# Optimization experiments

Measured on AMD Instinct MI355X. Metric: run time of the kernel, lower is better.

## Reference

```python
import jax, jax.numpy as jnp
import numpy as np

B, K_SLOTS, P = 4096, 8, 768
SLOT = P // 3          # 256, slot feature dim
HID = 256              # pres/up hidden width
NC, NP = 512, 512
LN_EPS = 1e-5


def _layernorm(x, g, b):
    m = jnp.mean(x, axis=-1, keepdims=True)
    v = jnp.var(x, axis=-1, keepdims=True)
    return (x - m) * jax.lax.rsqrt(v + LN_EPS) * g + b


def _mlp2(x, W1, b1, g, bt, W2, b2):
    # Linear -> LayerNorm -> ReLU -> Linear (torchvision ops.MLP with hidden=[256, out])
    h = jax.nn.relu(_layernorm(x @ W1 + b1, g, bt))
    return h @ W2 + b2


def setup_inputs() -> dict:
    key = jax.random.key(0)
    ks = jax.random.split(key, 24)
    rn = lambda k, shp, s=1.0: jax.random.normal(k, shp, dtype=jnp.float32) * s
    d = {
        "inst_embed": rn(ks[0], (B, P)),
        "slots": rn(ks[1], (B, K_SLOTS, SLOT)),
        # fc / fp: single Linear(p, p)
        "Wfc": rn(ks[2], (P, P), 1.0 / np.sqrt(P)),
        "bfc": jnp.zeros((P,), jnp.float32),
        "Wfp": rn(ks[3], (P, P), 1.0 / np.sqrt(P)),
        "bfp": jnp.zeros((P,), jnp.float32),
        # memory codebooks (plain randn per the original)
        "Kc": rn(ks[4], (NC, P)),
        "Vc": rn(ks[5], (NC, P)),
        "Kp": rn(ks[6], (NP, P)),
        "Vp": rn(ks[7], (NP, P)),
        # pres MLP: Linear(4p/3,256)+LN+ReLU, Linear(256,p/3)
        "pres_W1": rn(ks[8], (SLOT + P, HID), 1.0 / np.sqrt(SLOT + P)),
        "pres_b1": jnp.zeros((HID,), jnp.float32),
        "pres_g": jnp.ones((HID,), jnp.float32),
        "pres_bt": jnp.zeros((HID,), jnp.float32),
        "pres_W2": rn(ks[9], (HID, SLOT), 1.0 / np.sqrt(HID)),
        "pres_b2": jnp.zeros((SLOT,), jnp.float32),
        # up MLP: same shapes
        "up_W1": rn(ks[10], (SLOT + P, HID), 1.0 / np.sqrt(SLOT + P)),
        "up_b1": jnp.zeros((HID,), jnp.float32),
        "up_g": jnp.ones((HID,), jnp.float32),
        "up_bt": jnp.zeros((HID,), jnp.float32),
        "up_W2": rn(ks[11], (HID, SLOT), 1.0 / np.sqrt(HID)),
        "up_b2": jnp.zeros((SLOT,), jnp.float32),
    }
    return d


def reference(inst_embed, slots, Wfc, bfc, Wfp, bfp, Kc, Vc, Kp, Vp,
              pres_W1, pres_b1, pres_g, pres_bt, pres_W2, pres_b2,
              up_W1, up_b1, up_g, up_bt, up_W2, up_b2):
    scale = jnp.float32(np.sqrt(P))
    # selection: soft attention over the two codebooks
    Qc = inst_embed @ Wfc + bfc                     # [B, P]
    Qp = inst_embed @ Wfp + bfp                     # [B, P]
    c = jax.nn.softmax(jnp.einsum('bi,ci->bc', Qc, Kc) / scale, axis=-1) @ Vc  # [B, P]
    p = jax.nn.softmax(jnp.einsum('bi,pi->bp', Qp, Kp) / scale, axis=-1) @ Vp  # [B, P]
    # update: vectorized over the K slot loop of the original
    cb = jnp.broadcast_to(c[:, None, :], (B, K_SLOTS, P))
    pb = jnp.broadcast_to(p[:, None, :], (B, K_SLOTS, P))
    hc = jnp.concatenate([slots, cb], axis=-1)      # [B, K, SLOT+P]
    hp = jnp.concatenate([slots, pb], axis=-1)      # [B, K, SLOT+P]
    gate_pres = _mlp2(hc, pres_W1, pres_b1, pres_g, pres_bt, pres_W2, pres_b2)
    gate_up = _mlp2(hp, up_W1, up_b1, up_g, up_bt, up_W2, up_b2)
    return slots + gate_pres * gate_up              # [B, K, SLOT]
```

## Files before the change

kernel.cpp:

```cpp
#include <hip/hip_runtime.h>
#include <stdint.h>

#define BB    4096
#define KS    8
#define PP    768
#define SLOT  256
#define HID   256
#define NC    512
#define BKROWS (BB*KS)
typedef unsigned short u16;
typedef short bf16x8 __attribute__((ext_vector_type(8)));
typedef float f32x4  __attribute__((ext_vector_type(4)));

__device__ __forceinline__ u16 f2bf(float x) {
  union { float f; uint32_t u; } v; v.f = x;
  return (u16)((v.u + 0x7FFFu + ((v.u >> 16) & 1u)) >> 16);
}

__device__ __forceinline__ u16 f2h(float x) {
  union { _Float16 h; u16 u; } cv; cv.h = (_Float16)x; return cv.u;
}
__device__ __forceinline__ float h2f(u16 x) {
  union { u16 u; _Float16 h; } cv; cv.u = x; return (float)cv.h;
}

__device__ __forceinline__ void gload_lds16(u16* ldst, const u16* gsrc) {
  __builtin_amdgcn_global_load_lds(
      (const __attribute__((address_space(1))) void*)gsrc,
      (__attribute__((address_space(3))) void*)ldst, 16, 0, 0);
}

template<int EPI>
__device__ __forceinline__ void gemm_core6464(
    const u16* __restrict__ A, int lda,
    const u16* __restrict__ B, int ldb,
    const float* __restrict__ bias,
    void* __restrict__ out, int ldo, int K,
    int blockRow, int blockCol, u16* lsA, u16* lsB)
{
  const int tid  = threadIdx.x;
  const int w    = tid >> 6;
  const int lane = tid & 63;
  const int wm   = w >> 1, wn = w & 1;
  const int rl   = lane >> 4, cl = lane & 15;

  f32x4 acc[2][2];
  const f32x4 zero = {0.f, 0.f, 0.f, 0.f};
#pragma unroll
  for (int i = 0; i < 2; ++i)
#pragma unroll
    for (int j = 0; j < 2; ++j) acc[i][j] = zero;

  const u16* Ablk = A + (size_t)blockRow * lda;
  const u16* Bblk = B + (size_t)blockCol * ldb;

  for (int k0 = 0; k0 < K; k0 += 64) {
#pragma unroll
    for (int i = 0; i < 2; ++i) {
      int seg   = i * 4 + w;
      int off16 = seg * 64 + lane;
      int row   = off16 >> 3;
      int chunk = (off16 & 7) ^ (row & 7);
      gload_lds16(lsA + seg * 512, Ablk + (size_t)row * lda + k0 + chunk * 8);
    }
#pragma unroll
    for (int i = 0; i < 2; ++i) {
      int seg   = i * 4 + w;
      int off16 = seg * 64 + lane;
      int row   = off16 >> 3;
      int chunk = (off16 & 7) ^ (row & 7);
      gload_lds16(lsB + seg * 512, Bblk + (size_t)row * ldb + k0 + chunk * 8);
    }
    __syncthreads();

#pragma unroll
    for (int ks = 0; ks < 2; ++ks) {
      bf16x8 aF[2], bF[2];
#pragma unroll
      for (int f = 0; f < 2; ++f) {
        int r  = wm * 32 + f * 16 + cl;
        int ca = ((ks * 4 + rl) ^ (r & 7)) * 8;
        aF[f] = *(const bf16x8*)(lsA + r * 64 + ca);
        int rn = wn * 32 + f * 16 + cl;
        int cb = ((ks * 4 + rl) ^ (rn & 7)) * 8;
        bF[f] = *(const bf16x8*)(lsB + rn * 64 + cb);
      }
#pragma unroll
      for (int fm = 0; fm < 2; ++fm)
#pragma unroll
        for (int fn = 0; fn < 2; ++fn)
          acc[fm][fn] = __builtin_amdgcn_mfma_f32_16x16x32_bf16(
              aF[fm], bF[fn], acc[fm][fn], 0, 0, 0);
    }
    __syncthreads();
  }

#pragma unroll
  for (int fm = 0; fm < 2; ++fm) {
#pragma unroll
    for (int fn = 0; fn < 2; ++fn) {
      f32x4 v = acc[fm][fn];
#pragma unroll
      for (int r = 0; r < 4; ++r) {
        int grow = blockRow + wm * 32 + fm * 16 + rl * 4 + r;
        int gcol = blockCol + wn * 32 + fn * 16 + cl;
        float x = v[r];
        if constexpr (EPI == 2) {
          ((u16*)out)[(size_t)grow * ldo + gcol] = f2bf(x);
        } else if constexpr (EPI == 3) {
          x += bias[gcol];
          ((float*)out)[(size_t)grow * ldo + gcol] = x;
        } else if constexpr (EPI == 5) {
          x += bias[gcol];
          ((u16*)out)[(size_t)grow * ldo + gcol] = f2h(x);
        }
      }
    }
  }
}

__device__ __forceinline__ void cvt_seg(const float* __restrict__ in,
                                        u16* __restrict__ outp, int b, int n4) {
  int i = b * 256 + threadIdx.x;
  if (i < n4) {
    float4 v = ((const float4*)in)[i];
    ushort4 o;
    o.x = f2bf(v.x); o.y = f2bf(v.y); o.z = f2bf(v.z); o.w = f2bf(v.w);
    ((ushort4*)outp)[i] = o;
  }
}

__device__ __forceinline__ void pack_seg(const float* __restrict__ s0,
                                         const float* __restrict__ s1,
                                         u16* __restrict__ dst, int b) {
  int br = b >> 4, ng = b & 15;
  const float* src = br ? s1 : s0;
  int w = threadIdx.x >> 6, lane = threadIdx.x & 63;
  int rl = lane >> 4, cl = lane & 15;
#pragma unroll
  for (int s = 0; s < 2; ++s) {
    int step = w * 2 + s;
    union { u16 u[8]; uint4 q; } o;
#pragma unroll
    for (int j = 0; j < 8; ++j)
      o.u[j] = f2bf(src[(size_t)(step * 32 + rl * 8 + j) * 256 + ng * 16 + cl]);
    *(uint4*)(dst + (size_t)(((br * 16 + ng) * 8 + step) * 64 + lane) * 8) = o.q;
  }
}

__global__ __launch_bounds__(256) void prep_all(
    const float* __restrict__ inst, const float* __restrict__ Kc,
    const float* __restrict__ Kp, const float* __restrict__ Wfc,
    const float* __restrict__ Wfp, const float* __restrict__ Vc,
    const float* __restrict__ Vp, const float* __restrict__ pW1,
    const float* __restrict__ uW1, const float* __restrict__ pW2,
    const float* __restrict__ uW2, const float* __restrict__ bfc,
    const float* __restrict__ bfp,
    u16* instb, u16* Kcb, u16* Kpb, u16* Wfcb, u16* Wfpb, u16* Vcb, u16* Vpb,
    u16* W1Tp, u16* W1Tu, u16* W1pk, u16* W2pk, float* sb)
{
  __shared__ float tile[32][33];
  int b = blockIdx.x;
  if (b < 3072)      { cvt_seg(inst, instb, b,        786432); return; }
  else if (b < 3456) { cvt_seg(Kc,   Kcb,   b - 3072,  98304); return; }
  else if (b < 3840) { cvt_seg(Kp,   Kpb,   b - 3456,  98304); return; }
  else if (b < 4416) { cvt_seg(Wfc,  Wfcb,  b - 3840, 147456); return; }
  else if (b < 4992) { cvt_seg(Wfp,  Wfpb,  b - 4416, 147456); return; }
  else if (b < 5376) { cvt_seg(Vc,   Vcb,   b - 4992,  98304); return; }
  else if (b < 5760) { cvt_seg(Vp,   Vpb,   b - 5376,  98304); return; }
  else if (b < 6272) {
    int bb = b - 5760;
    const float* in = (bb < 256) ? pW1 : uW1;
    u16* outp = (bb < 256) ? W1Tp : W1Tu;
    bb &= 255;
    int tc = (bb & 7) * 32, tr = (bb >> 3) * 32;
    int lx = threadIdx.x & 31, ly = threadIdx.x >> 5;
#pragma unroll
    for (int i = 0; i < 32; i += 8)
      tile[ly + i][lx] = in[(size_t)(tr + ly + i) * 256 + tc + lx];
    __syncthreads();
#pragma unroll
    for (int i = 0; i < 32; i += 8)
      outp[(size_t)(tc + ly + i) * 1024 + tr + lx] = f2bf(tile[lx][ly + i]);
    return;
  }
  else if (b < 6304) { pack_seg(pW1, uW1, W1pk, b - 6272); return; }
  else if (b < 6336) { pack_seg(pW2, uW2, W2pk, b - 6304); return; }
  else {
    int w = threadIdx.x >> 6, lane = threadIdx.x & 63;
    int row = (b - 6336) * 4 + w;
    int br = row >> 9, n = row & 511;
    const float* Kr = (br ? Kp : Kc) + (size_t)n * PP;
    const float* bf = br ? bfp : bfc;
    float s = 0.f;
#pragma unroll
    for (int j = 0; j < 12; ++j) s += Kr[lane + j * 64] * bf[lane + j * 64];
#pragma unroll
    for (int o = 32; o; o >>= 1) s += __shfl_xor(s, o);
    if (!lane) sb[row] = s;
  }
}

__global__ __launch_bounds__(256) void gemm_mixed(
    const u16* Kcb, const u16* Kpb, const u16* Wfcb, const u16* Wfpb,
    u16* KWc, u16* KWp,
    const u16* W1Tp, const u16* W1Tu, const u16* Vcb, const u16* Vpb,
    u16* VW1p, u16* VW1u)
{
  __shared__ u16 lsA[64 * 64];
  __shared__ u16 lsB[64 * 64];
  int b = blockIdx.x;
  if (b < 192) {
    int z = b / 96, r = b % 96;
    gemm_core6464<2>(z ? Kpb : Kcb, PP, z ? Wfpb : Wfcb, PP, nullptr,
                     z ? KWp : KWc, PP, PP, (r & 7) * 64, (r >> 3) * 64, lsA, lsB);
  } else {
    int c = b - 192, z = c / 32, r = c % 32;
    gemm_core6464<2>((z ? W1Tu : W1Tp) + 256, 1024, z ? Vpb : Vcb, PP, nullptr,
                     z ? VW1u : VW1p, NC, PP, (r & 3) * 64, (r >> 2) * 64, lsA, lsB);
  }
}

__global__ __launch_bounds__(256) void gemm_scores(
    const u16* instb, const u16* KW, const float* sb, u16* scH)
{
  __shared__ u16 lsA[64 * 64];
  __shared__ u16 lsB[64 * 64];
  gemm_core6464<5>(instb, PP, KW, PP, sb, scH, 1024, PP,
                   blockIdx.x * 64, blockIdx.y * 64, lsA, lsB);
}

__global__ __launch_bounds__(256) void gemm_t(
    const u16* Pb, const u16* VW1p, const u16* VW1u,
    const float* pb1, const float* ub1, float* t0, float* t1)
{
  __shared__ u16 lsA[64 * 64];
  __shared__ u16 lsB[64 * 64];
  int z = blockIdx.z;
  gemm_core6464<3>(Pb + (size_t)z * BB * NC, NC, z ? VW1u : VW1p, NC,
                   z ? ub1 : pb1, z ? t1 : t0, SLOT, NC,
                   blockIdx.x * 64, blockIdx.y * 64, lsA, lsB);
}

__global__ __launch_bounds__(256) void softmax_rows(const u16* __restrict__ scH,
                                                    u16* __restrict__ Pp) {
  int w = threadIdx.x >> 6, lane = threadIdx.x & 63;
  int row = blockIdx.x * 4 + w;
  int i = row >> 1, b = row & 1;
  const u16* src = scH + (size_t)i * 1024 + b * 512 + lane * 8;
  uint4 q = *(const uint4*)src;
  const u16* hp = (const u16*)&q;
  float vv[8];
#pragma unroll
  for (int j = 0; j < 8; ++j) vv[j] = h2f(hp[j]);
  float m = vv[0];
#pragma unroll
  for (int j = 1; j < 8; ++j) m = fmaxf(m, vv[j]);
#pragma unroll
  for (int o = 32; o; o >>= 1) m = fmaxf(m, __shfl_xor(m, o));
  const float alpha = 0.03608439182435161f;
  float e[8], s = 0.f;
#pragma unroll
  for (int j = 0; j < 8; ++j) { e[j] = __expf((vv[j] - m) * alpha); s += e[j]; }
#pragma unroll
  for (int o = 32; o; o >>= 1) s += __shfl_xor(s, o);
  float inv = 1.f / s;
  union { u16 u[8]; uint4 q; } ou;
#pragma unroll
  for (int j = 0; j < 8; ++j) ou.u[j] = f2bf(e[j] * inv);
  *(uint4*)(Pp + ((size_t)b * BB + i) * 512 + lane * 8) = ou.q;
}

__global__ __launch_bounds__(512, 4) void fused_update(
    const float* __restrict__ slots,
    const float* __restrict__ t0, const float* __restrict__ t1,
    const u16* __restrict__ W1pk, const u16* __restrict__ W2pk,
    const float* __restrict__ pg, const float* __restrict__ pbt,
    const float* __restrict__ ug, const float* __restrict__ ubt,
    const float* __restrict__ pb2, const float* __restrict__ ub2,
    float* __restrict__ outp)
{
  __shared__ u16 lsH[2][32 * 256];
  __shared__ float lstat[2][32][16];
  __shared__ float lfin[2][32][2];

  const int tid = threadIdx.x, w = tid >> 6, lane = tid & 63;
  const int rl = lane >> 4, cl = lane & 15;
  const int blockRow = blockIdx.x * 32;

  u16* lsA = lsH[0];

#pragma unroll
  for (int it = 0; it < 4; ++it) {
    int L = it * 512 + tid;
    int row = L >> 6, qc = L & 63;
    float4 v = *(const float4*)(slots + (size_t)(blockRow + row) * 256 + qc * 4);
    ushort4 b; b.x = f2bf(v.x); b.y = f2bf(v.y); b.z = f2bf(v.z); b.w = f2bf(v.w);
    int chunk = qc >> 1, half = qc & 1;
    *(ushort4*)(lsA + row * 256 + (((chunk ^ (row & 7)) << 3) + half * 4)) = b;
  }

  float tp_[2][2], tu_[2][2];
#pragma unroll
  for (int fm = 0; fm < 2; ++fm) {
    size_t trr = (size_t)(blockIdx.x * 4 + fm * 2 + (rl >> 1)) * 256;
#pragma unroll
    for (int fn = 0; fn < 2; ++fn) {
      int col = w * 32 + fn * 16 + cl;
      tp_[fm][fn] = t0[trr + col];
      tu_[fm][fn] = t1[trr + col];
    }
  }

#define MF(A, B, C) C = __builtin_amdgcn_mfma_f32_16x16x32_bf16(A, B, C, 0, 0, 0);

  bf16x8 pb[3][2], ub[3][2];
#define FR1(NG, S) (*(const bf16x8*)(W1pk + (size_t)(((NG) * 8 + (S)) * 64 + lane) * 8))
#define LDW1(SL, S) { pb[SL][0] = FR1(w * 2, S);      pb[SL][1] = FR1(w * 2 + 1, S);  \
                      ub[SL][0] = FR1(16 + w * 2, S); ub[SL][1] = FR1(17 + w * 2, S); \
                      asm volatile("" ::: "memory"); }
  LDW1(0, 0) LDW1(1, 1) LDW1(2, 2)
  __syncthreads();

  f32x4 acc[2][4];
  const f32x4 zero = {0.f, 0.f, 0.f, 0.f};
#pragma unroll
  for (int i = 0; i < 2; ++i)
#pragma unroll
    for (int j = 0; j < 4; ++j) acc[i][j] = zero;

#pragma unroll
  for (int s = 0; s < 8; ++s) {
    const int sl = s % 3;
    bf16x8 a0 = *(const bf16x8*)(lsA + cl * 256 + (((s * 4 + rl) ^ (cl & 7)) << 3));
    bf16x8 a1 = *(const bf16x8*)(lsA + (16 + cl) * 256 + (((s * 4 + rl) ^ (cl & 7)) << 3));
    MF(a0, pb[sl][0], acc[0][0]) MF(a1, pb[sl][0], acc[1][0])
    MF(a0, pb[sl][1], acc[0][1]) MF(a1, pb[sl][1], acc[1][1])
    MF(a0, ub[sl][0], acc[0][2]) MF(a1, ub[sl][0], acc[1][2])
    MF(a0, ub[sl][1], acc[0][3]) MF(a1, ub[sl][1], acc[1][3])
    if (s < 5) LDW1(sl, s + 3)
  }
#undef LDW1
#undef FR1

#pragma unroll
  for (int fm = 0; fm < 2; ++fm)
#pragma unroll
    for (int fn = 0; fn < 2; ++fn)
#pragma unroll
      for (int r = 0; r < 4; ++r) {
        acc[fm][fn][r]     += tp_[fm][fn];
        acc[fm][2 + fn][r] += tu_[fm][fn];
      }

#pragma unroll
  for (int fm = 0; fm < 2; ++fm)
#pragma unroll
    for (int br = 0; br < 2; ++br) {
      f32x4 s = acc[fm][br * 2] + acc[fm][br * 2 + 1];
      f32x4 q = acc[fm][br * 2] * acc[fm][br * 2] + acc[fm][br * 2 + 1] * acc[fm][br * 2 + 1];
#pragma unroll
      for (int o = 1; o < 16; o <<= 1) {
#pragma unroll
        for (int r = 0; r < 4; ++r) {
          s[r] += __shfl_xor(s[r], o);
          q[r] += __shfl_xor(q[r], o);
        }
      }
      if (cl == 0) {
#pragma unroll
        for (int r = 0; r < 4; ++r) {
          int row = fm * 16 + rl * 4 + r;
          lstat[br][row][w]     = s[r];
          lstat[br][row][8 + w] = q[r];
        }
      }
    }
  __syncthreads();

  if (tid < 64) {
    int fb = tid >> 5, row = tid & 31;
    f32x4 a = *(const f32x4*)&lstat[fb][row][0];
    f32x4 b = *(const f32x4*)&lstat[fb][row][4];
    f32x4 c = *(const f32x4*)&lstat[fb][row][8];
    f32x4 d = *(const f32x4*)&lstat[fb][row][12];
    float ss = a[0] + a[1] + a[2] + a[3] + b[0] + b[1] + b[2] + b[3];
    float qq = c[0] + c[1] + c[2] + c[3] + d[0] + d[1] + d[2] + d[3];
    float mu = ss * (1.f / 256.f);
    lfin[fb][row][0] = mu;
    lfin[fb][row][1] = rsqrtf(qq * (1.f / 256.f) - mu * mu + 1e-5f);
  }
  __syncthreads();

  bf16x8 qp[3][2], qu[3][2];
#define FR2(NG, S) (*(const bf16x8*)(W2pk + (size_t)(((NG) * 8 + (S)) * 64 + lane) * 8))
#define LDW2(SL, S) { qp[SL][0] = FR2(w * 2, S);      qp[SL][1] = FR2(w * 2 + 1, S);  \
                      qu[SL][0] = FR2(16 + w * 2, S); qu[SL][1] = FR2(17 + w * 2, S); \
                      asm volatile("" ::: "memory"); }
  LDW2(0, 0)

  float b2p[2], b2u[2];
#pragma unroll
  for (int fn = 0; fn < 2; ++fn) {
    int col = w * 32 + fn * 16 + cl;
    b2p[fn] = pb2[col]; b2u[fn] = ub2[col];
  }

  {
    float gv[2][2], btv[2][2];
#pragma unroll
    for (int fn = 0; fn < 2; ++fn) {
      int col = w * 32 + fn * 16 + cl;
      gv[0][fn] = pg[col];  btv[0][fn] = pbt[col];
      gv[1][fn] = ug[col];  btv[1][fn] = ubt[col];
    }
#pragma unroll
    for (int fm = 0; fm < 2; ++fm) {
      float mean[2][4], rstd[2][4];
#pragma unroll
      for (int r = 0; r < 4; ++r) {
        int row = fm * 16 + rl * 4 + r;
        mean[0][r] = lfin[0][row][0]; rstd[0][r] = lfin[0][row][1];
        mean[1][r] = lfin[1][row][0]; rstd[1][r] = lfin[1][row][1];
      }
#pragma unroll
      for (int br = 0; br < 2; ++br)
#pragma unroll
        for (int fn = 0; fn < 2; ++fn) {
          int col = w * 32 + fn * 16 + cl;
#pragma unroll
          for (int r = 0; r < 4; ++r) {
            int row = fm * 16 + rl * 4 + r;
            float h = fmaxf((acc[fm][br * 2 + fn][r] - mean[br][r]) * rstd[br][r]
                            * gv[br][fn] + btv[br][fn], 0.f);
            lsH[br][row * 256 + (((col >> 3) ^ (row & 7)) << 3) + (col & 7)] = f2bf(h);
          }
        }
    }
  }
#pragma unroll
  for (int i = 0; i < 2; ++i)
#pragma unroll
    for (int j = 0; j < 4; ++j) acc[i][j] = zero;
  __syncthreads();

  LDW2(1, 1) LDW2(2, 2)
#pragma unroll
  for (int s = 0; s < 8; ++s) {
    const int sl = s % 3;
    bf16x8 aP0 = *(const bf16x8*)(lsH[0] + cl * 256 + (((s * 4 + rl) ^ (cl & 7)) << 3));
    bf16x8 aP1 = *(const bf16x8*)(lsH[0] + (16 + cl) * 256 + (((s * 4 + rl) ^ (cl & 7)) << 3));
    bf16x8 aU0 = *(const bf16x8*)(lsH[1] + cl * 256 + (((s * 4 + rl) ^ (cl & 7)) << 3));
    bf16x8 aU1 = *(const bf16x8*)(lsH[1] + (16 + cl) * 256 + (((s * 4 + rl) ^ (cl & 7)) << 3));
    MF(aP0, qp[sl][0], acc[0][0]) MF(aP1, qp[sl][0], acc[1][0])
    MF(aP0, qp[sl][1], acc[0][1]) MF(aP1, qp[sl][1], acc[1][1])
    MF(aU0, qu[sl][0], acc[0][2]) MF(aU1, qu[sl][0], acc[1][2])
    MF(aU0, qu[sl][1], acc[0][3]) MF(aU1, qu[sl][1], acc[1][3])
    if (s < 5) LDW2(sl, s + 3)
  }
#undef LDW2
#undef FR2
#undef MF

#pragma unroll
  for (int fm = 0; fm < 2; ++fm)
#pragma unroll
    for (int fn = 0; fn < 2; ++fn)
#pragma unroll
      for (int r = 0; r < 4; ++r) {
        float gp = acc[fm][fn][r]     + b2p[fn];
        float gu = acc[fm][2 + fn][r] + b2u[fn];
        int row = blockRow + fm * 16 + rl * 4 + r;
        int col = w * 32 + fn * 16 + cl;
        size_t idx = (size_t)row * 256 + col;
        outp[idx] = slots[idx] + gp * gu;
      }
}

extern "C" void kernel_launch(void* const* d_in, const int* in_sizes, int n_in,
                              void* d_out, int out_size, void* d_ws, size_t ws_size,
                              hipStream_t stream) {
  const float* inst  = (const float*)d_in[0];
  const float* slots = (const float*)d_in[1];
  const float* Wfc   = (const float*)d_in[2];
  const float* bfc   = (const float*)d_in[3];
  const float* Wfp   = (const float*)d_in[4];
  const float* bfp   = (const float*)d_in[5];
  const float* Kc    = (const float*)d_in[6];
  const float* Vc    = (const float*)d_in[7];
  const float* Kp    = (const float*)d_in[8];
  const float* Vp    = (const float*)d_in[9];
  const float* pW1   = (const float*)d_in[10];
  const float* pb1   = (const float*)d_in[11];
  const float* pg    = (const float*)d_in[12];
  const float* pbt   = (const float*)d_in[13];
  const float* pW2   = (const float*)d_in[14];
  const float* pb2   = (const float*)d_in[15];
  const float* uW1   = (const float*)d_in[16];
  const float* ub1   = (const float*)d_in[17];
  const float* ug    = (const float*)d_in[18];
  const float* ubt   = (const float*)d_in[19];
  const float* uW2   = (const float*)d_in[20];
  const float* ub2   = (const float*)d_in[21];
  float* out = (float*)d_out;
  char*  ws  = (char*)d_ws;

  const size_t OFF_INST  = 0;
  const size_t OFF_KC    = OFF_INST  + 6291456;
  const size_t OFF_KP    = OFF_KC    + 786432;
  const size_t OFF_WFCB  = OFF_KP    + 786432;
  const size_t OFF_WFPB  = OFF_WFCB  + 1179648;
  const size_t OFF_VCB   = OFF_WFPB  + 1179648;
  const size_t OFF_VPB   = OFF_VCB   + 786432;
  const size_t OFF_W1TP  = OFF_VPB   + 786432;
  const size_t OFF_W1TU  = OFF_W1TP  + 524288;
  const size_t OFF_W1PK  = OFF_W1TU  + 524288;
  const size_t OFF_W2PK  = OFF_W1PK  + 262144;
  const size_t OFF_KW    = OFF_W2PK  + 262144;
  const size_t OFF_VW1   = OFF_KW    + 1572864;
  const size_t OFF_SB    = OFF_VW1   + 524288;
  const size_t OFF_T     = OFF_SB    + 4096;
  const size_t OFF_SC    = OFF_T     + 8388608;
  const size_t OFF_P     = OFF_SC    + 8388608;

  u16*   instb = (u16*)(ws + OFF_INST);
  u16*   Kcb   = (u16*)(ws + OFF_KC);
  u16*   Kpb   = (u16*)(ws + OFF_KP);
  u16*   Wfcb  = (u16*)(ws + OFF_WFCB);
  u16*   Wfpb  = (u16*)(ws + OFF_WFPB);
  u16*   Vcb   = (u16*)(ws + OFF_VCB);
  u16*   Vpb   = (u16*)(ws + OFF_VPB);
  u16*   W1Tp  = (u16*)(ws + OFF_W1TP);
  u16*   W1Tu  = (u16*)(ws + OFF_W1TU);
  u16*   W1pk  = (u16*)(ws + OFF_W1PK);
  u16*   W2pk  = (u16*)(ws + OFF_W2PK);
  u16*   KWc   = (u16*)(ws + OFF_KW);
  u16*   KWp   = KWc + (size_t)NC * PP;
  u16*   VW1p  = (u16*)(ws + OFF_VW1);
  u16*   VW1u  = VW1p + (size_t)SLOT * NC;
  float* sb    = (float*)(ws + OFF_SB);
  float* t0    = (float*)(ws + OFF_T);
  float* t1    = t0 + (size_t)BB * SLOT;
  u16*   scH   = (u16*)(ws + OFF_SC);
  u16*   Pb    = (u16*)(ws + OFF_P);

  prep_all<<<dim3(6592), 256, 0, stream>>>(
      inst, Kc, Kp, Wfc, Wfp, Vc, Vp, pW1, uW1, pW2, uW2, bfc, bfp,
      instb, Kcb, Kpb, Wfcb, Wfpb, Vcb, Vpb, W1Tp, W1Tu, W1pk, W2pk, sb);

  gemm_mixed<<<dim3(256), 256, 0, stream>>>(
      Kcb, Kpb, Wfcb, Wfpb, KWc, KWp, W1Tp, W1Tu, Vcb, Vpb, VW1p, VW1u);

  gemm_scores<<<dim3(64, 16), 256, 0, stream>>>(instb, KWc, sb, scH);

  softmax_rows<<<dim3(2048), 256, 0, stream>>>(scH, Pb);

  gemm_t<<<dim3(64, 4, 2), 256, 0, stream>>>(Pb, VW1p, VW1u, pb1, ub1, t0, t1);

  fused_update<<<dim3(1024), 512, 0, stream>>>(
      slots, t0, t1, W1pk, W2pk, pg, pbt, ug, ubt, pb2, ub2, out);

  (void)in_sizes; (void)n_in; (void)out_size; (void)ws_size;
}
```

Before: 92.40 us.

## Split second MLP GEMM by branch across warps and combine gates via LDS

In the second-layer GEMM, each warp now handles one branch (pres or up) over 64 output columns instead of both branches over 32 columns. Each warp therefore reads A fragments from a single hidden buffer, which halves the LDS A-reads per MFMA. Pres-branch warps then write biased results to shared memory, and up-branch warps read them to form the gated residual output. This adds an extra barrier and an LDS round trip, and leaves half the warps idle during the final store.

Result: faster. 85.44 us (-7.5%).

```diff
diff --git a/kernel.cpp b/kernel.cpp
--- a/kernel.cpp
+++ b/kernel.cpp
@@ -392,19 +392,21 @@
   }
   __syncthreads();
 
-  bf16x8 qp[3][2], qu[3][2];
+  const int brw = w >> 2, wc = w & 3;
+  const u16* hsrc = lsH[brw];
+  const float* b2src = brw ? ub2 : pb2;
+  float b2v[4];
+#pragma unroll
+  for (int fn = 0; fn < 4; ++fn) b2v[fn] = b2src[wc * 64 + fn * 16 + cl];
+
+  bf16x8 bq[3][4];
 #define FR2(NG, S) (*(const bf16x8*)(W2pk + (size_t)(((NG) * 8 + (S)) * 64 + lane) * 8))
-#define LDW2(SL, S) { qp[SL][0] = FR2(w * 2, S);      qp[SL][1] = FR2(w * 2 + 1, S);  \
-                      qu[SL][0] = FR2(16 + w * 2, S); qu[SL][1] = FR2(17 + w * 2, S); \
+#define LDW2(SL, S) { bq[SL][0] = FR2(brw * 16 + wc * 4,     S); \
+                      bq[SL][1] = FR2(brw * 16 + wc * 4 + 1, S); \
+                      bq[SL][2] = FR2(brw * 16 + wc * 4 + 2, S); \
+                      bq[SL][3] = FR2(brw * 16 + wc * 4 + 3, S); \
                       asm volatile("" ::: "memory"); }
   LDW2(0, 0)
-
-  float b2p[2], b2u[2];
-#pragma unroll
-  for (int fn = 0; fn < 2; ++fn) {
-    int col = w * 32 + fn * 16 + cl;
-    b2p[fn] = pb2[col]; b2u[fn] = ub2[col];
-  }
 
   {
     float gv[2][2], btv[2][2];
@@ -448,33 +450,47 @@
 #pragma unroll
   for (int s = 0; s < 8; ++s) {
     const int sl = s % 3;
-    bf16x8 aP0 = *(const bf16x8*)(lsH[0] + cl * 256 + (((s * 4 + rl) ^ (cl & 7)) << 3));
-    bf16x8 aP1 = *(const bf16x8*)(lsH[0] + (16 + cl) * 256 + (((s * 4 + rl) ^ (cl & 7)) << 3));
-    bf16x8 aU0 = *(const bf16x8*)(lsH[1] + cl * 256 + (((s * 4 + rl) ^ (cl & 7)) << 3));
-    bf16x8 aU1 = *(const bf16x8*)(lsH[1] + (16 + cl) * 256 + (((s * 4 + rl) ^ (cl & 7)) << 3));
-    MF(aP0, qp[sl][0], acc[0][0]) MF(aP1, qp[sl][0], acc[1][0])
-    MF(aP0, qp[sl][1], acc[0][1]) MF(aP1, qp[sl][1], acc[1][1])
-    MF(aU0, qu[sl][0], acc[0][2]) MF(aU1, qu[sl][0], acc[1][2])
-    MF(aU0, qu[sl][1], acc[0][3]) MF(aU1, qu[sl][1], acc[1][3])
+    bf16x8 a0 = *(const bf16x8*)(hsrc + cl * 256 + (((s * 4 + rl) ^ (cl & 7)) << 3));
+    bf16x8 a1 = *(const bf16x8*)(hsrc + (16 + cl) * 256 + (((s * 4 + rl) ^ (cl & 7)) << 3));
+    MF(a0, bq[sl][0], acc[0][0]) MF(a1, bq[sl][0], acc[1][0])
+    MF(a0, bq[sl][1], acc[0][1]) MF(a1, bq[sl][1], acc[1][1])
+    MF(a0, bq[sl][2], acc[0][2]) MF(a1, bq[sl][2], acc[1][2])
+    MF(a0, bq[sl][3], acc[0][3]) MF(a1, bq[sl][3], acc[1][3])
     if (s < 5) LDW2(sl, s + 3)
   }
 #undef LDW2
 #undef FR2
 #undef MF
-
-#pragma unroll
-  for (int fm = 0; fm < 2; ++fm)
-#pragma unroll
-    for (int fn = 0; fn < 2; ++fn)
-#pragma unroll
-      for (int r = 0; r < 4; ++r) {
-        float gp = acc[fm][fn][r]     + b2p[fn];
-        float gu = acc[fm][2 + fn][r] + b2u[fn];
-        int row = blockRow + fm * 16 + rl * 4 + r;
-        int col = w * 32 + fn * 16 + cl;
-        size_t idx = (size_t)row * 256 + col;
-        outp[idx] = slots[idx] + gp * gu;
-      }
+  __syncthreads();
+
+  float* xbuf = (float*)&lsH[0][0];
+  const int base = wc * 2048;
+  if (brw == 0) {
+#pragma unroll
+    for (int fm = 0; fm < 2; ++fm)
+#pragma unroll
+      for (int fn = 0; fn < 4; ++fn)
+#pragma unroll
+        for (int r = 0; r < 4; ++r)
+          xbuf[base + ((fm * 4 + fn) * 4 + r) * 64 + lane] = acc[fm][fn][r] + b2v[fn];
+  }
+  __syncthreads();
+
+  if (brw == 1) {
+#pragma unroll
+    for (int fm = 0; fm < 2; ++fm)
+#pragma unroll
+      for (int fn = 0; fn < 4; ++fn)
+#pragma unroll
+        for (int r = 0; r < 4; ++r) {
+          float gp = xbuf[base + ((fm * 4 + fn) * 4 + r) * 64 + lane];
+          float gu = acc[fm][fn][r] + b2v[fn];
+          int row = blockRow + fm * 16 + rl * 4 + r;
+          int col = wc * 64 + fn * 16 + cl;
+          size_t idx = (size_t)row * 256 + col;
+          outp[idx] = slots[idx] + gp * gu;
+        }
+  }
 }
 
 extern "C" void kernel_launch(void* const* d_in, const int* in_sizes, int n_in,
```
